# Performance work log

Hardware: AMD Instinct MI355X
Metric: run time of the kernel (lower is better)

The kernel has to match this reference:

```python
import jax, jax.numpy as jnp
import numpy as np

N_NODES = 50000
N_COLORS = 256
D = 64
H = 128  # MLP hidden = 2*D
E_VV = 800000
E_VC = 400000


def _mlp_params(key, d_in, d_hid, d_out):
    k1, k2 = jax.random.split(key)
    s1 = 1.0 / np.sqrt(d_in)
    s2 = 1.0 / np.sqrt(d_hid)
    return (
        jax.random.uniform(k1, (d_in, d_hid), jnp.float32, -s1, s1),
        jnp.zeros((d_hid,), jnp.float32),
        jax.random.uniform(k2, (d_hid, d_out), jnp.float32, -s2, s2),
        jnp.zeros((d_out,), jnp.float32),
    )


def setup_inputs() -> dict:
    key = jax.random.key(0)
    ks = jax.random.split(key, 8)
    x_v = jax.random.normal(ks[0], (N_NODES, D), jnp.float32)
    x_c = jax.random.normal(ks[1], (N_COLORS, D), jnp.float32)
    src_vv = jax.random.randint(ks[2], (E_VV,), 0, N_NODES, jnp.int32)
    dst_vv = jax.random.randint(ks[3], (E_VV,), 0, N_NODES, jnp.int32)
    src_vc = jax.random.randint(ks[4], (E_VC,), 0, N_COLORS, jnp.int32)
    dst_vc = jax.random.randint(ks[5], (E_VC,), 0, N_NODES, jnp.int32)
    W1v, b1v, W2v, b2v = _mlp_params(ks[6], D, H, D)
    W1c, b1c, W2c, b2c = _mlp_params(ks[7], D, H, D)
    return {
        "x_v": x_v, "x_c": x_c,
        "W1v": W1v, "b1v": b1v, "W2v": W2v, "b2v": b2v,
        "W1c": W1c, "b1c": b1c, "W2c": W2c, "b2c": b2c,
        "src_vv": src_vv, "dst_vv": dst_vv,
        "src_vc": src_vc, "dst_vc": dst_vc,
    }


def reference(x_v, x_c, W1v, b1v, W2v, b2v, W1c, b1c, W2c, b2c,
              src_vv, dst_vv, src_vc, dst_vc):
    n = x_v.shape[0]
    # vertex->vertex messages: gather, MLP, scatter-sum
    mv = jax.nn.relu(x_v[src_vv] @ W1v + b1v) @ W2v + b2v  # [E_vv, D]
    agg_v = jax.ops.segment_sum(mv, dst_vv, num_segments=n)
    # color->vertex messages: gather color embeddings, MLP, scatter-sum
    mc = jax.nn.relu(x_c[src_vc] @ W1c + b1c) @ W2c + b2c  # [E_vc, D]
    agg_c = jax.ops.segment_sum(mc, dst_vc, num_segments=n)
    return jax.nn.relu(x_v + agg_v + agg_c)
```

## Files before the change

kernel.cpp:

```cpp
#include <hip/hip_runtime.h>

#define NN 50000
#define NC 256
#define DD 64
#define HH 128
#define EVV 800000
#define EVC 400000
#define NE 1200000
#define NB 196
#define BCAP 8192
#define MLPV_B 782
#define MLPC_B 4
#define MLP_B (MLPV_B + MLPC_B)
#define FILL_EPB 2048
#define FILL_B 586
#define QUADS 197
#define K1_B (QUADS * 7)
#define GAT_B (NB * 8)
#define VCAP 64
#define HROW 136

typedef __attribute__((ext_vector_type(8))) short bf16x8;
typedef __attribute__((ext_vector_type(4))) float f32x4;

__device__ __forceinline__ unsigned short f2bf(float x) {
  unsigned u = __float_as_uint(x);
  u = (u + 0x7fffu + ((u >> 16) & 1u)) >> 16;
  return (unsigned short)u;
}

union SMem {
  unsigned short hl[4][16 * HROW];
  struct {
    int cnt[NB];
    int off[NB];
    int gbase[NB];
    int sa[256], sb[256];
    unsigned int stage[FILL_EPB];
  } f;
};

__global__ __launch_bounds__(256) void prep_kernel(
    const float* __restrict__ W1v, const float* __restrict__ W2v,
    const float* __restrict__ W1c, const float* __restrict__ W2c,
    unsigned short* __restrict__ wt) {
  const int tid = blockIdx.x * 256 + threadIdx.x;
  const int sel = tid >> 13;
  const int t = tid & 8191;
  unsigned short* dst = wt + sel * 8192;
  if (sel == 0) {
    const int n = t >> 6, k = t & 63;
    dst[t] = f2bf(W1v[k * HH + n]);
  } else if (sel == 1) {
    const int n = t >> 7, k = t & 127;
    dst[t] = f2bf(W2v[k * DD + n]);
  } else if (sel == 2) {
    const int n = t >> 6, k = t & 63;
    dst[t] = f2bf(W1c[k * HH + n]);
  } else {
    const int n = t >> 7, k = t & 127;
    dst[t] = f2bf(W2c[k * DD + n]);
  }
}

__device__ __forceinline__ void mlp_mfma(
    const float* __restrict__ X, const unsigned short* __restrict__ W1t,
    const float* __restrict__ b1, const unsigned short* __restrict__ W2t,
    const float* __restrict__ b2, unsigned short* __restrict__ Y, int blk,
    int nrows, unsigned short* __restrict__ hl) {
  const int lane = threadIdx.x & 63;
  const int m = lane & 15;
  const int quad = lane >> 4;
  const int rowbase = blk * 64 + (threadIdx.x >> 6) * 16;

  bf16x8 a0, a1;
  {
    float4 xa = {0.f, 0.f, 0.f, 0.f}, xb = xa, xc = xa, xd = xa;
    const int row = rowbase + m;
    if (row < nrows) {
      const float* xp = X + (size_t)row * DD + quad * 8;
      xa = *(const float4*)(xp);
      xb = *(const float4*)(xp + 4);
      xc = *(const float4*)(xp + 32);
      xd = *(const float4*)(xp + 36);
    }
    a0[0] = (short)f2bf(xa.x); a0[1] = (short)f2bf(xa.y);
    a0[2] = (short)f2bf(xa.z); a0[3] = (short)f2bf(xa.w);
    a0[4] = (short)f2bf(xb.x); a0[5] = (short)f2bf(xb.y);
    a0[6] = (short)f2bf(xb.z); a0[7] = (short)f2bf(xb.w);
    a1[0] = (short)f2bf(xc.x); a1[1] = (short)f2bf(xc.y);
    a1[2] = (short)f2bf(xc.z); a1[3] = (short)f2bf(xc.w);
    a1[4] = (short)f2bf(xd.x); a1[5] = (short)f2bf(xd.y);
    a1[6] = (short)f2bf(xd.z); a1[7] = (short)f2bf(xd.w);
  }

#pragma unroll
  for (int nt = 0; nt < 8; ++nt) {
    const int n = nt * 16 + m;
    const float bv = b1[n];
    f32x4 acc = {bv, bv, bv, bv};
    const bf16x8 b0 = *(const bf16x8*)(W1t + n * 64 + quad * 8);
    const bf16x8 b1f = *(const bf16x8*)(W1t + n * 64 + 32 + quad * 8);
    acc = __builtin_amdgcn_mfma_f32_16x16x32_bf16(a0, b0, acc, 0, 0, 0);
    acc = __builtin_amdgcn_mfma_f32_16x16x32_bf16(a1, b1f, acc, 0, 0, 0);
#pragma unroll
    for (int r = 0; r < 4; ++r)
      hl[(quad * 4 + r) * HROW + n] = f2bf(fmaxf(acc[r], 0.f));
  }

  bf16x8 ha[4];
#pragma unroll
  for (int kc = 0; kc < 4; ++kc)
    ha[kc] = *(const bf16x8*)(hl + m * HROW + kc * 32 + quad * 8);

#pragma unroll
  for (int nt = 0; nt < 4; ++nt) {
    const int n = nt * 16 + m;
    const float bv = b2[n];
    f32x4 acc = {bv, bv, bv, bv};
#pragma unroll
    for (int kc = 0; kc < 4; ++kc) {
      const bf16x8 bw = *(const bf16x8*)(W2t + n * 128 + kc * 32 + quad * 8);
      acc = __builtin_amdgcn_mfma_f32_16x16x32_bf16(ha[kc], bw, acc, 0, 0, 0);
    }
#pragma unroll
    for (int r = 0; r < 4; ++r) {
      const int row = rowbase + quad * 4 + r;
      if (row < nrows) Y[(size_t)row * DD + n] = f2bf(acc[r]);
    }
  }
}

__device__ __forceinline__ void fill_block(
    const int* __restrict__ src_vv, const int* __restrict__ dst_vv,
    const int* __restrict__ src_vc, const int* __restrict__ dst_vc,
    int* __restrict__ gcur, unsigned int* __restrict__ records, int blk,
    SMem* sm) {
  const int t = threadIdx.x;
  const int base = blk * FILL_EPB;
  if (t < NB) sm->f.cnt[t] = 0;
  __syncthreads();

  unsigned int rec[8];
  int rk[8];
#pragma unroll
  for (int r = 0; r < 8; ++r) {
    const int e = base + r * 256 + t;
    rk[r] = -1;
    if (e < NE) {
      int s, d;
      if (e < EVV) {
        s = src_vv[e];
        d = dst_vv[e];
      } else {
        s = NN + src_vc[e - EVV];
        d = dst_vc[e - EVV];
      }
      rec[r] = ((unsigned int)d << 16) | (unsigned int)s;
      rk[r] = atomicAdd(&sm->f.cnt[d >> 8], 1);
    }
  }
  __syncthreads();

  const int val = (t < NB) ? sm->f.cnt[t] : 0;
  sm->f.sa[t] = val;
  __syncthreads();
  int* s = sm->f.sa;
  int* d = sm->f.sb;
  for (int o = 1; o < 256; o <<= 1) {
    d[t] = s[t] + ((t >= o) ? s[t - o] : 0);
    __syncthreads();
    int* tmp = s; s = d; d = tmp;
  }
  if (t < NB) {
    sm->f.off[t] = s[t] - val;
    sm->f.gbase[t] = t * BCAP + ((val > 0) ? atomicAdd(&gcur[t], val) : 0);
  }
  __syncthreads();

#pragma unroll
  for (int r = 0; r < 8; ++r)
    if (rk[r] >= 0) sm->f.stage[sm->f.off[rec[r] >> 24] + rk[r]] = rec[r];
  __syncthreads();

  const int total = (NE - base < FILL_EPB) ? (NE - base) : FILL_EPB;
  for (int i = t; i < total; i += 256) {
    const unsigned int u = sm->f.stage[i];
    const int b2 = u >> 24;
    records[sm->f.gbase[b2] + (i - sm->f.off[b2])] = u;
  }
}

__global__ __launch_bounds__(256) void k1_kernel(
    const float* __restrict__ x_v, const float* __restrict__ x_c,
    const float* __restrict__ b1v, const float* __restrict__ b2v,
    const float* __restrict__ b1c, const float* __restrict__ b2c,
    const unsigned short* __restrict__ wt,
    const int* __restrict__ src_vv, const int* __restrict__ dst_vv,
    const int* __restrict__ src_vc, const int* __restrict__ dst_vc,
    unsigned short* __restrict__ table, int* __restrict__ gcur,
    unsigned int* __restrict__ records) {
  __shared__ SMem sm;
  const int q = blockIdx.x / 7;
  const int r = blockIdx.x % 7;
  if (r < 3) {
    const int fid = q * 3 + r;
    if (fid >= FILL_B) return;
    fill_block(src_vv, dst_vv, src_vc, dst_vc, gcur, records, fid, &sm);
  } else {
    const int mb = q * 4 + (r - 3);
    if (mb >= MLP_B) return;
    unsigned short* hl = sm.hl[threadIdx.x >> 6];
    if (mb < MLPV_B)
      mlp_mfma(x_v, wt, b1v, wt + 8192, b2v, table, mb, NN, hl);
    else
      mlp_mfma(x_c, wt + 16384, b1c, wt + 24576, b2c,
               table + (size_t)NN * DD, mb - MLPV_B, NC, hl);
  }
}

__device__ __forceinline__ void acc8(float* a, const uint4 t) {
  a[0] += __uint_as_float(t.x << 16);
  a[1] += __uint_as_float(t.x & 0xffff0000u);
  a[2] += __uint_as_float(t.y << 16);
  a[3] += __uint_as_float(t.y & 0xffff0000u);
  a[4] += __uint_as_float(t.z << 16);
  a[5] += __uint_as_float(t.z & 0xffff0000u);
  a[6] += __uint_as_float(t.w << 16);
  a[7] += __uint_as_float(t.w & 0xffff0000u);
}

__device__ __forceinline__ void place(unsigned int u, int sub, int* c1,
                                      unsigned short* slots) {
  const int dd = u >> 16;
  if (((dd >> 5) & 7) == sub) {
    const int lv = dd & 31;
    const int pos = atomicAdd(&c1[lv], 1);
    if (pos < VCAP) slots[lv * VCAP + pos] = (unsigned short)(u & 0xffffu);
  }
}

__global__ __launch_bounds__(256) void gather_kernel(
    const uint4* __restrict__ table4, const unsigned int* __restrict__ records,
    const int* __restrict__ gcur, const float4* __restrict__ xv4,
    float4* __restrict__ out4) {
  __shared__ int c1[32];
  __shared__ unsigned short slots[32 * VCAP];
  const int t = threadIdx.x;
  const int bucket = blockIdx.x >> 3;
  const int sub = blockIdx.x & 7;
  const int start = bucket * BCAP;
  const int nrec = gcur[bucket];

  const int g = t >> 3;
  const int c = t & 7;
  const int v = bucket * 256 + sub * 32 + g;
  const size_t ob = (size_t)v * 16 + c * 2;
  float4 x0 = {0.f, 0.f, 0.f, 0.f}, x1 = x0;
  if (v < NN) {
    x0 = xv4[ob];
    x1 = xv4[ob + 1];
  }

  if (t < 32) c1[t] = 0;
  __syncthreads();

  const uint4* rec4 = (const uint4*)(records + start);
  const int nfull = nrec >> 2;
  for (int q = t; q < nfull; q += 256) {
    const uint4 u = rec4[q];
    place(u.x, sub, c1, slots);
    place(u.y, sub, c1, slots);
    place(u.z, sub, c1, slots);
    place(u.w, sub, c1, slots);
  }
  for (int j = (nfull << 2) + t; j < nrec; j += 256)
    place(records[start + j], sub, c1, slots);
  __syncthreads();

  if (v >= NN) return;
  int n = c1[g];
  n = (n > VCAP) ? VCAP : n;
  const unsigned short* sl = slots + g * VCAP;

  float a[8];
#pragma unroll
  for (int r = 0; r < 8; ++r) a[r] = 0.f;

  int i = 0;
  for (; i + 8 <= n; i += 8) {
    const int e0 = sl[i + 0];
    const int e1 = sl[i + 1];
    const int e2 = sl[i + 2];
    const int e3 = sl[i + 3];
    const int e4 = sl[i + 4];
    const int e5 = sl[i + 5];
    const int e6 = sl[i + 6];
    const int e7 = sl[i + 7];
    const uint4 t0 = table4[(size_t)e0 * 8 + c];
    const uint4 t1 = table4[(size_t)e1 * 8 + c];
    const uint4 t2 = table4[(size_t)e2 * 8 + c];
    const uint4 t3 = table4[(size_t)e3 * 8 + c];
    const uint4 t4 = table4[(size_t)e4 * 8 + c];
    const uint4 t5 = table4[(size_t)e5 * 8 + c];
    const uint4 t6 = table4[(size_t)e6 * 8 + c];
    const uint4 t7 = table4[(size_t)e7 * 8 + c];
    acc8(a, t0); acc8(a, t1); acc8(a, t2); acc8(a, t3);
    acc8(a, t4); acc8(a, t5); acc8(a, t6); acc8(a, t7);
  }
  for (; i + 4 <= n; i += 4) {
    const int e0 = sl[i + 0];
    const int e1 = sl[i + 1];
    const int e2 = sl[i + 2];
    const int e3 = sl[i + 3];
    const uint4 t0 = table4[(size_t)e0 * 8 + c];
    const uint4 t1 = table4[(size_t)e1 * 8 + c];
    const uint4 t2 = table4[(size_t)e2 * 8 + c];
    const uint4 t3 = table4[(size_t)e3 * 8 + c];
    acc8(a, t0); acc8(a, t1); acc8(a, t2); acc8(a, t3);
  }
  for (; i < n; ++i) {
    const uint4 t0 = table4[(size_t)sl[i] * 8 + c];
    acc8(a, t0);
  }

  float4 o0, o1;
  o0.x = fmaxf(x0.x + a[0], 0.f);
  o0.y = fmaxf(x0.y + a[1], 0.f);
  o0.z = fmaxf(x0.z + a[2], 0.f);
  o0.w = fmaxf(x0.w + a[3], 0.f);
  o1.x = fmaxf(x1.x + a[4], 0.f);
  o1.y = fmaxf(x1.y + a[5], 0.f);
  o1.z = fmaxf(x1.z + a[6], 0.f);
  o1.w = fmaxf(x1.w + a[7], 0.f);
  out4[ob] = o0;
  out4[ob + 1] = o1;
}

extern "C" void kernel_launch(void* const* d_in, const int* in_sizes, int n_in,
                              void* d_out, int out_size, void* d_ws,
                              size_t ws_size, hipStream_t stream) {
  const float* x_v = (const float*)d_in[0];
  const float* x_c = (const float*)d_in[1];
  const float* W1v = (const float*)d_in[2];
  const float* b1v = (const float*)d_in[3];
  const float* W2v = (const float*)d_in[4];
  const float* b2v = (const float*)d_in[5];
  const float* W1c = (const float*)d_in[6];
  const float* b1c = (const float*)d_in[7];
  const float* W2c = (const float*)d_in[8];
  const float* b2c = (const float*)d_in[9];
  const int* src_vv = (const int*)d_in[10];
  const int* dst_vv = (const int*)d_in[11];
  const int* src_vc = (const int*)d_in[12];
  const int* dst_vc = (const int*)d_in[13];
  float* out = (float*)d_out;

  char* p = (char*)d_ws;
  unsigned short* table = (unsigned short*)p;
  p += (size_t)(NN + NC) * DD * sizeof(unsigned short);
  unsigned int* records = (unsigned int*)p;
  p += (size_t)NB * BCAP * sizeof(unsigned int);
  unsigned short* wt = (unsigned short*)p;
  p += (size_t)4 * 8192 * sizeof(unsigned short);
  int* gcur = (int*)p;

  hipMemsetAsync(gcur, 0, NB * sizeof(int), stream);

  prep_kernel<<<128, 256, 0, stream>>>(W1v, W2v, W1c, W2c, wt);

  k1_kernel<<<K1_B, 256, 0, stream>>>(x_v, x_c, b1v, b2v, b1c, b2c, wt,
                                      src_vv, dst_vv, src_vc, dst_vc, table,
                                      gcur, records);

  gather_kernel<<<GAT_B, 256, 0, stream>>>((const uint4*)table, records, gcur,
                                           (const float4*)x_v, (float4*)out);
}
```

Measured before the change: 145.8 us.

## Replace bucketed record sort with direct per-vertex global slot lists

Drops the two-level bucketing: the fill blocks no longer stage records by 256-vertex bucket in shared memory, and the gather blocks no longer rescan whole buckets to build per-vertex slot lists. Each edge now does one global atomicAdd on a per-destination counter and writes its source index straight into a per-vertex slot array. Gather reads the counter and slots directly with vectorized index loads. The counter reset moves from a memset into the prep kernel. This removes the redundant 8x bucket rescans in gather and the shared-memory prefix scan, at the cost of 1.2M scattered global atomics and scattered 2-byte writes.

```diff
diff --git a/kernel.cpp b/kernel.cpp
--- a/kernel.cpp
+++ b/kernel.cpp
@@ -7,17 +7,15 @@
 #define EVV 800000
 #define EVC 400000
 #define NE 1200000
-#define NB 196
-#define BCAP 8192
+#define VCAP 64
 #define MLPV_B 782
 #define MLPC_B 4
 #define MLP_B (MLPV_B + MLPC_B)
-#define FILL_EPB 2048
-#define FILL_B 586
+#define PLACE_EPB 2048
+#define PLACE_B 586
 #define QUADS 197
 #define K1_B (QUADS * 7)
-#define GAT_B (NB * 8)
-#define VCAP 64
+#define GAT_B 1563
 #define HROW 136
 
 typedef __attribute__((ext_vector_type(8))) short bf16x8;
@@ -29,37 +27,29 @@
   return (unsigned short)u;
 }
 
-union SMem {
-  unsigned short hl[4][16 * HROW];
-  struct {
-    int cnt[NB];
-    int off[NB];
-    int gbase[NB];
-    int sa[256], sb[256];
-    unsigned int stage[FILL_EPB];
-  } f;
-};
-
 __global__ __launch_bounds__(256) void prep_kernel(
     const float* __restrict__ W1v, const float* __restrict__ W2v,
     const float* __restrict__ W1c, const float* __restrict__ W2c,
-    unsigned short* __restrict__ wt) {
+    unsigned short* __restrict__ wt, int* __restrict__ cnt) {
   const int tid = blockIdx.x * 256 + threadIdx.x;
-  const int sel = tid >> 13;
-  const int t = tid & 8191;
-  unsigned short* dst = wt + sel * 8192;
-  if (sel == 0) {
-    const int n = t >> 6, k = t & 63;
-    dst[t] = f2bf(W1v[k * HH + n]);
-  } else if (sel == 1) {
-    const int n = t >> 7, k = t & 127;
-    dst[t] = f2bf(W2v[k * DD + n]);
-  } else if (sel == 2) {
-    const int n = t >> 6, k = t & 63;
-    dst[t] = f2bf(W1c[k * HH + n]);
-  } else {
-    const int n = t >> 7, k = t & 127;
-    dst[t] = f2bf(W2c[k * DD + n]);
+  if (tid < NN) cnt[tid] = 0;
+  if (tid < 32768) {
+    const int sel = tid >> 13;
+    const int t = tid & 8191;
+    unsigned short* dst = wt + sel * 8192;
+    if (sel == 0) {
+      const int n = t >> 6, k = t & 63;
+      dst[t] = f2bf(W1v[k * HH + n]);
+    } else if (sel == 1) {
+      const int n = t >> 7, k = t & 127;
+      dst[t] = f2bf(W2v[k * DD + n]);
+    } else if (sel == 2) {
+      const int n = t >> 6, k = t & 63;
+      dst[t] = f2bf(W1c[k * HH + n]);
+    } else {
+      const int n = t >> 7, k = t & 127;
+      dst[t] = f2bf(W2c[k * DD + n]);
+    }
   }
 }
 
@@ -131,63 +121,33 @@
   }
 }
 
-__device__ __forceinline__ void fill_block(
+__device__ __forceinline__ void place_block(
     const int* __restrict__ src_vv, const int* __restrict__ dst_vv,
     const int* __restrict__ src_vc, const int* __restrict__ dst_vc,
-    int* __restrict__ gcur, unsigned int* __restrict__ records, int blk,
-    SMem* sm) {
+    int* __restrict__ cnt, unsigned short* __restrict__ slotg, int blk) {
   const int t = threadIdx.x;
-  const int base = blk * FILL_EPB;
-  if (t < NB) sm->f.cnt[t] = 0;
-  __syncthreads();
-
-  unsigned int rec[8];
-  int rk[8];
+  const int base = blk * PLACE_EPB;
+  int ss[8], dd[8];
 #pragma unroll
   for (int r = 0; r < 8; ++r) {
     const int e = base + r * 256 + t;
-    rk[r] = -1;
+    ss[r] = -1;
     if (e < NE) {
-      int s, d;
       if (e < EVV) {
-        s = src_vv[e];
-        d = dst_vv[e];
+        ss[r] = src_vv[e];
+        dd[r] = dst_vv[e];
       } else {
-        s = NN + src_vc[e - EVV];
-        d = dst_vc[e - EVV];
+        ss[r] = NN + src_vc[e - EVV];
+        dd[r] = dst_vc[e - EVV];
       }
-      rec[r] = ((unsigned int)d << 16) | (unsigned int)s;
-      rk[r] = atomicAdd(&sm->f.cnt[d >> 8], 1);
-    }
-  }
-  __syncthreads();
-
-  const int val = (t < NB) ? sm->f.cnt[t] : 0;
-  sm->f.sa[t] = val;
-  __syncthreads();
-  int* s = sm->f.sa;
-  int* d = sm->f.sb;
-  for (int o = 1; o < 256; o <<= 1) {
-    d[t] = s[t] + ((t >= o) ? s[t - o] : 0);
-    __syncthreads();
-    int* tmp = s; s = d; d = tmp;
-  }
-  if (t < NB) {
-    sm->f.off[t] = s[t] - val;
-    sm->f.gbase[t] = t * BCAP + ((val > 0) ? atomicAdd(&gcur[t], val) : 0);
-  }
-  __syncthreads();
-
-#pragma unroll
-  for (int r = 0; r < 8; ++r)
-    if (rk[r] >= 0) sm->f.stage[sm->f.off[rec[r] >> 24] + rk[r]] = rec[r];
-  __syncthreads();
-
-  const int total = (NE - base < FILL_EPB) ? (NE - base) : FILL_EPB;
-  for (int i = t; i < total; i += 256) {
-    const unsigned int u = sm->f.stage[i];
-    const int b2 = u >> 24;
-    records[sm->f.gbase[b2] + (i - sm->f.off[b2])] = u;
+    }
+  }
+#pragma unroll
+  for (int r = 0; r < 8; ++r) {
+    if (ss[r] >= 0) {
+      const int pos = atomicAdd(&cnt[dd[r]], 1);
+      if (pos < VCAP) slotg[dd[r] * VCAP + pos] = (unsigned short)ss[r];
+    }
   }
 }
 
@@ -198,19 +158,19 @@
     const unsigned short* __restrict__ wt,
     const int* __restrict__ src_vv, const int* __restrict__ dst_vv,
     const int* __restrict__ src_vc, const int* __restrict__ dst_vc,
-    unsigned short* __restrict__ table, int* __restrict__ gcur,
-    unsigned int* __restrict__ records) {
-  __shared__ SMem sm;
+    unsigned short* __restrict__ table, int* __restrict__ cnt,
+    unsigned short* __restrict__ slotg) {
+  __shared__ unsigned short hl4[4][16 * HROW];
   const int q = blockIdx.x / 7;
   const int r = blockIdx.x % 7;
   if (r < 3) {
     const int fid = q * 3 + r;
-    if (fid >= FILL_B) return;
-    fill_block(src_vv, dst_vv, src_vc, dst_vc, gcur, records, fid, &sm);
+    if (fid >= PLACE_B) return;
+    place_block(src_vv, dst_vv, src_vc, dst_vc, cnt, slotg, fid);
   } else {
     const int mb = q * 4 + (r - 3);
     if (mb >= MLP_B) return;
-    unsigned short* hl = sm.hl[threadIdx.x >> 6];
+    unsigned short* hl = hl4[threadIdx.x >> 6];
     if (mb < MLPV_B)
       mlp_mfma(x_v, wt, b1v, wt + 8192, b2v, table, mb, NN, hl);
     else
@@ -230,58 +190,21 @@
   a[7] += __uint_as_float(t.w & 0xffff0000u);
 }
 
-__device__ __forceinline__ void place(unsigned int u, int sub, int* c1,
-                                      unsigned short* slots) {
-  const int dd = u >> 16;
-  if (((dd >> 5) & 7) == sub) {
-    const int lv = dd & 31;
-    const int pos = atomicAdd(&c1[lv], 1);
-    if (pos < VCAP) slots[lv * VCAP + pos] = (unsigned short)(u & 0xffffu);
-  }
-}
-
 __global__ __launch_bounds__(256) void gather_kernel(
-    const uint4* __restrict__ table4, const unsigned int* __restrict__ records,
-    const int* __restrict__ gcur, const float4* __restrict__ xv4,
+    const uint4* __restrict__ table4, const int* __restrict__ cnt,
+    const unsigned short* __restrict__ slotg, const float4* __restrict__ xv4,
     float4* __restrict__ out4) {
-  __shared__ int c1[32];
-  __shared__ unsigned short slots[32 * VCAP];
   const int t = threadIdx.x;
-  const int bucket = blockIdx.x >> 3;
-  const int sub = blockIdx.x & 7;
-  const int start = bucket * BCAP;
-  const int nrec = gcur[bucket];
-
   const int g = t >> 3;
   const int c = t & 7;
-  const int v = bucket * 256 + sub * 32 + g;
+  const int v = blockIdx.x * 32 + g;
+  if (v >= NN) return;
   const size_t ob = (size_t)v * 16 + c * 2;
-  float4 x0 = {0.f, 0.f, 0.f, 0.f}, x1 = x0;
-  if (v < NN) {
-    x0 = xv4[ob];
-    x1 = xv4[ob + 1];
-  }
-
-  if (t < 32) c1[t] = 0;
-  __syncthreads();
-
-  const uint4* rec4 = (const uint4*)(records + start);
-  const int nfull = nrec >> 2;
-  for (int q = t; q < nfull; q += 256) {
-    const uint4 u = rec4[q];
-    place(u.x, sub, c1, slots);
-    place(u.y, sub, c1, slots);
-    place(u.z, sub, c1, slots);
-    place(u.w, sub, c1, slots);
-  }
-  for (int j = (nfull << 2) + t; j < nrec; j += 256)
-    place(records[start + j], sub, c1, slots);
-  __syncthreads();
-
-  if (v >= NN) return;
-  int n = c1[g];
+  const float4 x0 = xv4[ob];
+  const float4 x1 = xv4[ob + 1];
+  int n = cnt[v];
   n = (n > VCAP) ? VCAP : n;
-  const unsigned short* sl = slots + g * VCAP;
+  const unsigned short* sl = slotg + v * VCAP;
 
   float a[8];
 #pragma unroll
@@ -289,14 +212,15 @@
 
   int i = 0;
   for (; i + 8 <= n; i += 8) {
-    const int e0 = sl[i + 0];
-    const int e1 = sl[i + 1];
-    const int e2 = sl[i + 2];
-    const int e3 = sl[i + 3];
-    const int e4 = sl[i + 4];
-    const int e5 = sl[i + 5];
-    const int e6 = sl[i + 6];
-    const int e7 = sl[i + 7];
+    const uint4 sv = *(const uint4*)(sl + i);
+    const int e0 = sv.x & 0xffff;
+    const int e1 = sv.x >> 16;
+    const int e2 = sv.y & 0xffff;
+    const int e3 = sv.y >> 16;
+    const int e4 = sv.z & 0xffff;
+    const int e5 = sv.z >> 16;
+    const int e6 = sv.w & 0xffff;
+    const int e7 = sv.w >> 16;
     const uint4 t0 = table4[(size_t)e0 * 8 + c];
     const uint4 t1 = table4[(size_t)e1 * 8 + c];
     const uint4 t2 = table4[(size_t)e2 * 8 + c];
@@ -308,16 +232,18 @@
     acc8(a, t0); acc8(a, t1); acc8(a, t2); acc8(a, t3);
     acc8(a, t4); acc8(a, t5); acc8(a, t6); acc8(a, t7);
   }
-  for (; i + 4 <= n; i += 4) {
-    const int e0 = sl[i + 0];
-    const int e1 = sl[i + 1];
-    const int e2 = sl[i + 2];
-    const int e3 = sl[i + 3];
+  if (i + 4 <= n) {
+    const uint2 sv = *(const uint2*)(sl + i);
+    const int e0 = sv.x & 0xffff;
+    const int e1 = sv.x >> 16;
+    const int e2 = sv.y & 0xffff;
+    const int e3 = sv.y >> 16;
     const uint4 t0 = table4[(size_t)e0 * 8 + c];
     const uint4 t1 = table4[(size_t)e1 * 8 + c];
     const uint4 t2 = table4[(size_t)e2 * 8 + c];
     const uint4 t3 = table4[(size_t)e3 * 8 + c];
     acc8(a, t0); acc8(a, t1); acc8(a, t2); acc8(a, t3);
+    i += 4;
   }
   for (; i < n; ++i) {
     const uint4 t0 = table4[(size_t)sl[i] * 8 + c];
@@ -359,20 +285,18 @@
   char* p = (char*)d_ws;
   unsigned short* table = (unsigned short*)p;
   p += (size_t)(NN + NC) * DD * sizeof(unsigned short);
-  unsigned int* records = (unsigned int*)p;
-  p += (size_t)NB * BCAP * sizeof(unsigned int);
+  unsigned short* slotg = (unsigned short*)p;
+  p += (size_t)NN * VCAP * sizeof(unsigned short);
   unsigned short* wt = (unsigned short*)p;
   p += (size_t)4 * 8192 * sizeof(unsigned short);
-  int* gcur = (int*)p;
-
-  hipMemsetAsync(gcur, 0, NB * sizeof(int), stream);
-
-  prep_kernel<<<128, 256, 0, stream>>>(W1v, W2v, W1c, W2c, wt);
+  int* cnt = (int*)p;
+
+  prep_kernel<<<256, 256, 0, stream>>>(W1v, W2v, W1c, W2c, wt, cnt);
 
   k1_kernel<<<K1_B, 256, 0, stream>>>(x_v, x_c, b1v, b2v, b1c, b2c, wt,
                                       src_vv, dst_vv, src_vc, dst_vc, table,
-                                      gcur, records);
-
-  gather_kernel<<<GAT_B, 256, 0, stream>>>((const uint4*)table, records, gcur,
+                                      cnt, slotg);
+
+  gather_kernel<<<GAT_B, 256, 0, stream>>>((const uint4*)table, cnt, slotg,
                                            (const float4*)x_v, (float4*)out);
 }
```

Result: slower. 179.6 us (+23.2%).

## Gather one bucket per 1024-thread block and fold gcur reset into prep

Applied to the files above, without the earlier changes.

The gather kernel now uses one 1024-thread block per bucket instead of eight 256-thread sub-blocks. Previously each sub-block scanned the whole bucket's record list and kept only its 32 vertices, so each bucket was read eight times; now it is scanned once and each thread handles two vertices. The separate memset of the bucket counters moves into prep_kernel, dropping one stream operation. The trade-off is fewer blocks (196) with larger LDS use (about 33 KB each), which may cut occupancy and latency hiding for the random table gathers.

```diff
diff --git a/kernel.cpp b/kernel.cpp
--- a/kernel.cpp
+++ b/kernel.cpp
@@ -16,7 +16,6 @@
 #define FILL_B 586
 #define QUADS 197
 #define K1_B (QUADS * 7)
-#define GAT_B (NB * 8)
 #define VCAP 64
 #define HROW 136
 
@@ -43,8 +42,9 @@
 __global__ __launch_bounds__(256) void prep_kernel(
     const float* __restrict__ W1v, const float* __restrict__ W2v,
     const float* __restrict__ W1c, const float* __restrict__ W2c,
-    unsigned short* __restrict__ wt) {
+    unsigned short* __restrict__ wt, int* __restrict__ gcur) {
   const int tid = blockIdx.x * 256 + threadIdx.x;
+  if (tid < NB) gcur[tid] = 0;
   const int sel = tid >> 13;
   const int t = tid & 8191;
   unsigned short* dst = wt + sel * 8192;
@@ -230,111 +230,106 @@
   a[7] += __uint_as_float(t.w & 0xffff0000u);
 }
 
-__device__ __forceinline__ void place(unsigned int u, int sub, int* c1,
+__device__ __forceinline__ void place(unsigned int u, int* c1,
                                       unsigned short* slots) {
-  const int dd = u >> 16;
-  if (((dd >> 5) & 7) == sub) {
-    const int lv = dd & 31;
-    const int pos = atomicAdd(&c1[lv], 1);
-    if (pos < VCAP) slots[lv * VCAP + pos] = (unsigned short)(u & 0xffffu);
-  }
-}
-
-__global__ __launch_bounds__(256) void gather_kernel(
+  const int lv = (u >> 16) & 255;
+  const int pos = atomicAdd(&c1[lv], 1);
+  if (pos < VCAP) slots[lv * VCAP + pos] = (unsigned short)(u & 0xffffu);
+}
+
+__global__ __launch_bounds__(1024) void gather_kernel(
     const uint4* __restrict__ table4, const unsigned int* __restrict__ records,
     const int* __restrict__ gcur, const float4* __restrict__ xv4,
     float4* __restrict__ out4) {
-  __shared__ int c1[32];
-  __shared__ unsigned short slots[32 * VCAP];
+  __shared__ int c1[256];
+  __shared__ unsigned short slots[256 * VCAP];
   const int t = threadIdx.x;
-  const int bucket = blockIdx.x >> 3;
-  const int sub = blockIdx.x & 7;
+  const int bucket = blockIdx.x;
   const int start = bucket * BCAP;
   const int nrec = gcur[bucket];
 
+  if (t < 256) c1[t] = 0;
+  __syncthreads();
+
+  const uint4* rec4 = (const uint4*)(records + start);
+  const int nfull = nrec >> 2;
+  for (int q = t; q < nfull; q += 1024) {
+    const uint4 u = rec4[q];
+    place(u.x, c1, slots);
+    place(u.y, c1, slots);
+    place(u.z, c1, slots);
+    place(u.w, c1, slots);
+  }
+  for (int j = (nfull << 2) + t; j < nrec; j += 1024)
+    place(records[start + j], c1, slots);
+  __syncthreads();
+
   const int g = t >> 3;
   const int c = t & 7;
-  const int v = bucket * 256 + sub * 32 + g;
-  const size_t ob = (size_t)v * 16 + c * 2;
-  float4 x0 = {0.f, 0.f, 0.f, 0.f}, x1 = x0;
-  if (v < NN) {
-    x0 = xv4[ob];
-    x1 = xv4[ob + 1];
-  }
-
-  if (t < 32) c1[t] = 0;
-  __syncthreads();
-
-  const uint4* rec4 = (const uint4*)(records + start);
-  const int nfull = nrec >> 2;
-  for (int q = t; q < nfull; q += 256) {
-    const uint4 u = rec4[q];
-    place(u.x, sub, c1, slots);
-    place(u.y, sub, c1, slots);
-    place(u.z, sub, c1, slots);
-    place(u.w, sub, c1, slots);
-  }
-  for (int j = (nfull << 2) + t; j < nrec; j += 256)
-    place(records[start + j], sub, c1, slots);
-  __syncthreads();
-
-  if (v >= NN) return;
-  int n = c1[g];
-  n = (n > VCAP) ? VCAP : n;
-  const unsigned short* sl = slots + g * VCAP;
-
-  float a[8];
-#pragma unroll
-  for (int r = 0; r < 8; ++r) a[r] = 0.f;
-
-  int i = 0;
-  for (; i + 8 <= n; i += 8) {
-    const int e0 = sl[i + 0];
-    const int e1 = sl[i + 1];
-    const int e2 = sl[i + 2];
-    const int e3 = sl[i + 3];
-    const int e4 = sl[i + 4];
-    const int e5 = sl[i + 5];
-    const int e6 = sl[i + 6];
-    const int e7 = sl[i + 7];
-    const uint4 t0 = table4[(size_t)e0 * 8 + c];
-    const uint4 t1 = table4[(size_t)e1 * 8 + c];
-    const uint4 t2 = table4[(size_t)e2 * 8 + c];
-    const uint4 t3 = table4[(size_t)e3 * 8 + c];
-    const uint4 t4 = table4[(size_t)e4 * 8 + c];
-    const uint4 t5 = table4[(size_t)e5 * 8 + c];
-    const uint4 t6 = table4[(size_t)e6 * 8 + c];
-    const uint4 t7 = table4[(size_t)e7 * 8 + c];
-    acc8(a, t0); acc8(a, t1); acc8(a, t2); acc8(a, t3);
-    acc8(a, t4); acc8(a, t5); acc8(a, t6); acc8(a, t7);
-  }
-  for (; i + 4 <= n; i += 4) {
-    const int e0 = sl[i + 0];
-    const int e1 = sl[i + 1];
-    const int e2 = sl[i + 2];
-    const int e3 = sl[i + 3];
-    const uint4 t0 = table4[(size_t)e0 * 8 + c];
-    const uint4 t1 = table4[(size_t)e1 * 8 + c];
-    const uint4 t2 = table4[(size_t)e2 * 8 + c];
-    const uint4 t3 = table4[(size_t)e3 * 8 + c];
-    acc8(a, t0); acc8(a, t1); acc8(a, t2); acc8(a, t3);
-  }
-  for (; i < n; ++i) {
-    const uint4 t0 = table4[(size_t)sl[i] * 8 + c];
-    acc8(a, t0);
-  }
-
-  float4 o0, o1;
-  o0.x = fmaxf(x0.x + a[0], 0.f);
-  o0.y = fmaxf(x0.y + a[1], 0.f);
-  o0.z = fmaxf(x0.z + a[2], 0.f);
-  o0.w = fmaxf(x0.w + a[3], 0.f);
-  o1.x = fmaxf(x1.x + a[4], 0.f);
-  o1.y = fmaxf(x1.y + a[5], 0.f);
-  o1.z = fmaxf(x1.z + a[6], 0.f);
-  o1.w = fmaxf(x1.w + a[7], 0.f);
-  out4[ob] = o0;
-  out4[ob + 1] = o1;
+  for (int p = 0; p < 2; ++p) {
+    const int lv = p * 128 + g;
+    const int v = bucket * 256 + lv;
+    if (v >= NN) continue;
+    const size_t ob = (size_t)v * 16 + c * 2;
+    const float4 x0 = xv4[ob];
+    const float4 x1 = xv4[ob + 1];
+    int n = c1[lv];
+    n = (n > VCAP) ? VCAP : n;
+    const unsigned short* sl = slots + lv * VCAP;
+
+    float a[8];
+#pragma unroll
+    for (int r = 0; r < 8; ++r) a[r] = 0.f;
+
+    int i = 0;
+    for (; i + 8 <= n; i += 8) {
+      const int e0 = sl[i + 0];
+      const int e1 = sl[i + 1];
+      const int e2 = sl[i + 2];
+      const int e3 = sl[i + 3];
+      const int e4 = sl[i + 4];
+      const int e5 = sl[i + 5];
+      const int e6 = sl[i + 6];
+      const int e7 = sl[i + 7];
+      const uint4 t0 = table4[(size_t)e0 * 8 + c];
+      const uint4 t1 = table4[(size_t)e1 * 8 + c];
+      const uint4 t2 = table4[(size_t)e2 * 8 + c];
+      const uint4 t3 = table4[(size_t)e3 * 8 + c];
+      const uint4 t4 = table4[(size_t)e4 * 8 + c];
+      const uint4 t5 = table4[(size_t)e5 * 8 + c];
+      const uint4 t6 = table4[(size_t)e6 * 8 + c];
+      const uint4 t7 = table4[(size_t)e7 * 8 + c];
+      acc8(a, t0); acc8(a, t1); acc8(a, t2); acc8(a, t3);
+      acc8(a, t4); acc8(a, t5); acc8(a, t6); acc8(a, t7);
+    }
+    for (; i + 4 <= n; i += 4) {
+      const int e0 = sl[i + 0];
+      const int e1 = sl[i + 1];
+      const int e2 = sl[i + 2];
+      const int e3 = sl[i + 3];
+      const uint4 t0 = table4[(size_t)e0 * 8 + c];
+      const uint4 t1 = table4[(size_t)e1 * 8 + c];
+      const uint4 t2 = table4[(size_t)e2 * 8 + c];
+      const uint4 t3 = table4[(size_t)e3 * 8 + c];
+      acc8(a, t0); acc8(a, t1); acc8(a, t2); acc8(a, t3);
+    }
+    for (; i < n; ++i) {
+      const uint4 t0 = table4[(size_t)sl[i] * 8 + c];
+      acc8(a, t0);
+    }
+
+    float4 o0, o1;
+    o0.x = fmaxf(x0.x + a[0], 0.f);
+    o0.y = fmaxf(x0.y + a[1], 0.f);
+    o0.z = fmaxf(x0.z + a[2], 0.f);
+    o0.w = fmaxf(x0.w + a[3], 0.f);
+    o1.x = fmaxf(x1.x + a[4], 0.f);
+    o1.y = fmaxf(x1.y + a[5], 0.f);
+    o1.z = fmaxf(x1.z + a[6], 0.f);
+    o1.w = fmaxf(x1.w + a[7], 0.f);
+    out4[ob] = o0;
+    out4[ob + 1] = o1;
+  }
 }
 
 extern "C" void kernel_launch(void* const* d_in, const int* in_sizes, int n_in,
@@ -365,14 +360,12 @@
   p += (size_t)4 * 8192 * sizeof(unsigned short);
   int* gcur = (int*)p;
 
-  hipMemsetAsync(gcur, 0, NB * sizeof(int), stream);
-
-  prep_kernel<<<128, 256, 0, stream>>>(W1v, W2v, W1c, W2c, wt);
+  prep_kernel<<<128, 256, 0, stream>>>(W1v, W2v, W1c, W2c, wt, gcur);
 
   k1_kernel<<<K1_B, 256, 0, stream>>>(x_v, x_c, b1v, b2v, b1c, b2c, wt,
                                       src_vv, dst_vv, src_vc, dst_vc, table,
                                       gcur, records);
 
-  gather_kernel<<<GAT_B, 256, 0, stream>>>((const uint4*)table, records, gcur,
-                                           (const float4*)x_v, (float4*)out);
-}
+  gather_kernel<<<NB, 1024, 0, stream>>>((const uint4*)table, records, gcur,
+                                         (const float4*)x_v, (float4*)out);
+}
```

New measurement: 139.0 us. 1.05x faster.
